# Kernel optimization log

Measured on AMD Instinct MI355X. Metric: run time of the kernel, lower is better.

## Reference

```python
import jax, jax.numpy as jnp
import numpy as np

B, D = 64, 65536   # batch, num default boxes
NEG_POS = 3        # negative:positive mining ratio (init arg)


def _bce_with_logits(x, t):
    # numerically stable elementwise BCE-with-logits (matches torch)
    return jnp.maximum(x, 0.0) - x * t + jnp.log1p(jnp.exp(-jnp.abs(x)))


def _smooth_l1(d):
    ad = jnp.abs(d)
    return jnp.where(ad < 1.0, 0.5 * d * d, ad - 0.5)


def setup_inputs() -> dict:
    key = jax.random.key(0)
    k1, k2, k3, k4 = jax.random.split(key, 4)
    loc_data = jax.random.normal(k1, (B, D, 4), dtype=jnp.float32)
    conf_data = jax.random.normal(k2, (B, D, 1), dtype=jnp.float32)
    loc_t = jax.random.normal(k3, (B, D, 4), dtype=jnp.float32)
    conf_t = (jax.random.uniform(k4, (B, D)) < 0.02).astype(jnp.int32)
    return {"loc_data": loc_data, "conf_data": conf_data,
            "loc_t": loc_t, "conf_t": conf_t}


def reference(loc_data, conf_data, loc_t, conf_t):
    pos = conf_t > 0                                  # [B, D]
    num_pos = pos.sum(axis=1, keepdims=True)          # [B, 1]

    # ---- localization loss: smooth-L1 mean over positive box coords ----
    pf = pos[:, :, None].astype(loc_data.dtype)       # [B, D, 1]
    sl1 = _smooth_l1(loc_data - loc_t) * pf           # [B, D, 4]
    n_loc_elems = pf.sum() * 4.0                      # masked-gather -> mean
    loss_l = sl1.sum() / n_loc_elems

    # ---- confidence loss with hard negative mining ----
    logits = conf_data[:, :, 0]                       # [B, D]
    bce = _bce_with_logits(logits, conf_t.astype(logits.dtype))
    bce_neg = jnp.where(pos, 0.0, bce)                # zero-out positives
    # double argsort -> per-row rank of each element's loss (descending)
    loss_idx = jnp.argsort(-bce_neg, axis=1)          # [B, D]
    idx_rank = jnp.argsort(loss_idx, axis=1)          # [B, D]
    num_neg = jnp.minimum(num_pos * NEG_POS, D)       # [B, 1]
    neg = idx_rank < num_neg                          # top-k hardest negatives
    sel = (pos | neg).astype(logits.dtype)            # [B, D]
    loss_c = (bce * sel).sum() / sel.sum()            # mean over selected

    N = num_pos.sum().astype(logits.dtype)
    return (loss_l / N, loss_c / N)
```

## Files before the change

### kernel.cpp

```cpp
#include <hip/hip_runtime.h>
#include <stdint.h>


#define B_ 64
#define D_ 65536
#define NEGPOS 3
#define BPR 16
#define NBLK (B_ * BPR)
#define CHUNK (D_ / BPR)
#define XC 1.25f
#define HBINS 4096
#define XRANGE 5.0f
#define CJCAP 1024

#define OFF_SL1P     0
#define OFF_BCEP     8192
#define OFF_NP       16384
#define OFF_CC       20480
#define OFF_NEGSUM   24576
#define OFF_KSEL     25088
#define OFF_CNT      25344
#define OFF_CAND     32768

__device__ __forceinline__ void stgF(float* p, float v) {
    __hip_atomic_store(p, v, __ATOMIC_RELAXED, __HIP_MEMORY_SCOPE_AGENT);
}
__device__ __forceinline__ void stgU(unsigned* p, unsigned v) {
    __hip_atomic_store(p, v, __ATOMIC_RELAXED, __HIP_MEMORY_SCOPE_AGENT);
}
__device__ __forceinline__ void stgI(int* p, int v) {
    __hip_atomic_store(p, v, __ATOMIC_RELAXED, __HIP_MEMORY_SCOPE_AGENT);
}
__device__ __forceinline__ void stgD(double* p, double v) {
    __hip_atomic_store(p, v, __ATOMIC_RELAXED, __HIP_MEMORY_SCOPE_AGENT);
}
__device__ __forceinline__ float ldgF(const float* p) {
    return __hip_atomic_load(p, __ATOMIC_RELAXED, __HIP_MEMORY_SCOPE_AGENT);
}
__device__ __forceinline__ unsigned ldgU(const unsigned* p) {
    return __hip_atomic_load(p, __ATOMIC_RELAXED, __HIP_MEMORY_SCOPE_AGENT);
}
__device__ __forceinline__ int ldgI(const int* p) {
    return __hip_atomic_load(p, __ATOMIC_RELAXED, __HIP_MEMORY_SCOPE_AGENT);
}
__device__ __forceinline__ double ldgD(const double* p) {
    return __hip_atomic_load(p, __ATOMIC_RELAXED, __HIP_MEMORY_SCOPE_AGENT);
}

__device__ __forceinline__ float softplus_f(float x) {
    return fmaxf(x, 0.0f) + log1pf(expf(-fabsf(x)));
}

__device__ __forceinline__ int bin_of_x(float x) {
    int b = (int)((x - XC) * ((float)HBINS / XRANGE));
    return max(0, min(HBINS - 1, b));
}

__device__ __forceinline__ float smooth_l1_4(float4 a, float4 b) {
    float s = 0.0f, d, ad;
    d = a.x - b.x; ad = fabsf(d); s += (ad < 1.0f) ? 0.5f * d * d : ad - 0.5f;
    d = a.y - b.y; ad = fabsf(d); s += (ad < 1.0f) ? 0.5f * d * d : ad - 0.5f;
    d = a.z - b.z; ad = fabsf(d); s += (ad < 1.0f) ? 0.5f * d * d : ad - 0.5f;
    d = a.w - b.w; ad = fabsf(d); s += (ad < 1.0f) ? 0.5f * d * d : ad - 0.5f;
    return s;
}

__device__ __forceinline__ double wredD(double v) {
#pragma unroll
    for (int o = 32; o > 0; o >>= 1) v += __shfl_down(v, o, 64);
    return v;
}
__device__ __forceinline__ int wredI(int v) {
#pragma unroll
    for (int o = 32; o > 0; o >>= 1) v += __shfl_down(v, o, 64);
    return v;
}

__device__ __forceinline__ int blockSumI(int v, int* sh) {
    int w = wredI(v);
    const int lane = threadIdx.x & 63, wid = threadIdx.x >> 6;
    __syncthreads();
    if (lane == 0) sh[wid] = w;
    __syncthreads();
    return sh[0] + sh[1] + sh[2] + sh[3];
}

__global__ void __launch_bounds__(256)
mbl_fused(const float4* __restrict__ loc4, const float* __restrict__ conf,
          const float4* __restrict__ loct4, const int* __restrict__ conft,
          unsigned char* __restrict__ ws, float* __restrict__ out)
{
    __shared__ union {
        struct { float lcand[CHUNK]; unsigned short lpos[CHUNK]; } a;
        struct { unsigned hist[HBINS]; float ubuf[CJCAP]; } b;
    } u;
    __shared__ unsigned wtot[4];
    __shared__ double wr[8];
    __shared__ double wrC[4];
    __shared__ int shN[4], shK[4];
    __shared__ unsigned segoff[BPR + 1], sccS[BPR], wsuf[4];
    __shared__ unsigned shJ, shRemJ, shCj, shNP;
    __shared__ int shI[4];
    __shared__ int shLast;

    const int block = blockIdx.x;
    const int row = block >> 4;
    const int base = block * CHUNK;
    const int lane = threadIdx.x & 63, wid = threadIdx.x >> 6;

    {
        const float4* c4 = (const float4*)(conf + base);
        const int4*   t4 = (const int4*)(conft + base);

        float4 xv[4]; int4 tv[4];
#pragma unroll
        for (int it = 0; it < 4; it++) {
            const int g = threadIdx.x + it * 256;
            xv[it] = c4[g];
            tv[it] = t4[g];
        }

        double bcp = 0.0;
        unsigned cntc = 0, cntp = 0;
#pragma unroll
        for (int it = 0; it < 4; it++) {
#pragma unroll
            for (int c = 0; c < 4; c++) {
                float x = (c == 0) ? xv[it].x : (c == 1) ? xv[it].y : (c == 2) ? xv[it].z : xv[it].w;
                int   t = (c == 0) ? tv[it].x : (c == 1) ? tv[it].y : (c == 2) ? tv[it].z : tv[it].w;
                if (t > 0) { cntp++; bcp += (double)(softplus_f(x) - x); }
                else if (x >= XC) cntc++;
            }
        }

        unsigned pk = (cntc << 16) | cntp;
        unsigned incl = pk;
#pragma unroll
        for (int o = 1; o < 64; o <<= 1) {
            unsigned v = __shfl_up(incl, o, 64);
            if (lane >= o) incl += v;
        }
        unsigned excl = incl - pk;
        if (lane == 63) wtot[wid] = incl;
        __syncthreads();
        unsigned wbase = 0;
        for (int w = 0; w < wid; w++) wbase += wtot[w];
        const unsigned tot = wtot[0] + wtot[1] + wtot[2] + wtot[3];
        const unsigned totc = tot >> 16, totp = tot & 0xFFFFu;
        unsigned offc = (excl >> 16) + (wbase >> 16);
        unsigned offp = (excl & 0xFFFFu) + (wbase & 0xFFFFu);

#pragma unroll
        for (int it = 0; it < 4; it++) {
#pragma unroll
            for (int c = 0; c < 4; c++) {
                float x = (c == 0) ? xv[it].x : (c == 1) ? xv[it].y : (c == 2) ? xv[it].z : xv[it].w;
                int   t = (c == 0) ? tv[it].x : (c == 1) ? tv[it].y : (c == 2) ? tv[it].z : tv[it].w;
                const int li = (threadIdx.x + it * 256) * 4 + c;
                if (t > 0) u.a.lpos[offp++] = (unsigned short)li;
                else if (x >= XC) u.a.lcand[offc++] = x;
            }
        }
        __syncthreads();

        float* seg = (float*)(ws + OFF_CAND) + (size_t)block * CHUNK;
        for (unsigned i = threadIdx.x; i < totc; i += 256) stgF(seg + i, u.a.lcand[i]);

        double sl1 = 0.0;
        for (unsigned i = threadIdx.x; i < totp; i += 256) {
            const int e = base + (int)u.a.lpos[i];
            sl1 += (double)smooth_l1_4(loc4[e], loct4[e]);
        }

        double s1 = wredD(sl1), s2 = wredD(bcp);
        if (lane == 0) { wr[wid] = s1; wr[4 + wid] = s2; }
        __syncthreads();
        if (threadIdx.x == 0) {
            stgD((double*)(ws + OFF_SL1P) + block, wr[0] + wr[1] + wr[2] + wr[3]);
            stgD((double*)(ws + OFF_BCEP) + block, wr[4] + wr[5] + wr[6] + wr[7]);
            stgU((unsigned*)(ws + OFF_NP) + block, totp);
            stgU((unsigned*)(ws + OFF_CC) + block, totc);
        }
    }

    __syncthreads();
    if (threadIdx.x == 0) {
        unsigned old = __hip_atomic_fetch_add(
            (unsigned*)(ws + OFF_CNT) + row, 1u,
            __ATOMIC_RELAXED, __HIP_MEMORY_SCOPE_AGENT);
        shLast = (old == BPR - 1) ? 1 : 0;
    }
    __syncthreads();
    if (!shLast) return;

    const unsigned* ccp = (const unsigned*)(ws + OFF_CC) + row * BPR;
    const unsigned* npp = (const unsigned*)(ws + OFF_NP) + row * BPR;

    if (wid == 0) {
        unsigned c = (lane < BPR) ? ldgU(ccp + lane) : 0u;
        unsigned p = (lane < BPR) ? ldgU(npp + lane) : 0u;
        unsigned inc = c;
#pragma unroll
        for (int o = 1; o < BPR; o <<= 1) {
            unsigned v = __shfl_up(inc, o, 64);
            if (lane >= o) inc += v;
        }
        unsigned ptot = p;
#pragma unroll
        for (int o = 1; o < BPR; o <<= 1) ptot += __shfl_down(ptot, o, 64);
        if (lane < BPR) { segoff[lane] = inc - c; sccS[lane] = c; }
        if (lane == BPR - 1) segoff[BPR] = inc;
        if (lane == 0) { shNP = ptot; shCj = 0; }
    }
    __syncthreads();

    const int np = (int)shNP;
    const unsigned n = segoff[BPR];
    long long k = (long long)np * NEGPOS;
    if (k > D_) k = D_;
    long long negs = (long long)D_ - np;
    if (k > negs) k = negs;
    if (threadIdx.x == 0) stgI((int*)(ws + OFF_KSEL) + row, (int)k);

    bool donesum = false;
    bool needfb = false;
    if (k <= 0) {
        if (threadIdx.x == 0) stgD((double*)(ws + OFF_NEGSUM) + row, 0.0);
        donesum = true;
    } else if ((long long)n < k) {
        needfb = true;
    }

    const float* cand = (const float*)(ws + OFF_CAND);

    if (!donesum && !needfb) {
        for (int i = threadIdx.x; i < HBINS; i += 256) u.b.hist[i] = 0;
        __syncthreads();
        const int s = threadIdx.x >> 4, li = threadIdx.x & 15;
        const float* gseg = cand + (size_t)(row * BPR + s) * CHUNK;
        const unsigned cs = sccS[s];
        for (unsigned i = li; i < cs; i += 16)
            atomicAdd(&u.b.hist[bin_of_x(ldgF(gseg + i))], 1u);
        __syncthreads();

        {
            unsigned s16 = 0; const int b0 = threadIdx.x * 16;
#pragma unroll
            for (int i = 0; i < 16; i++) s16 += u.b.hist[b0 + i];
            unsigned suf = s16;
#pragma unroll
            for (int o = 1; o < 64; o <<= 1) {
                unsigned v = __shfl_down(suf, o, 64);
                if (lane + o < 64) suf += v;
            }
            if (lane == 0) wsuf[wid] = suf;
            __syncthreads();
            unsigned add = 0;
            for (int w = wid + 1; w < 4; w++) add += wsuf[w];
            suf += add;
            const unsigned sufx = suf - s16;
            if ((long long)sufx < k && (long long)suf >= k) {
                long long cum = sufx;
                for (int b = b0 + 15; b >= b0; b--) {
                    cum += u.b.hist[b];
                    if (cum >= k) {
                        shJ = (unsigned)b;
                        shRemJ = (unsigned)(k - (cum - (long long)u.b.hist[b]));
                        break;
                    }
                }
            }
        }
        __syncthreads();
        const unsigned J = shJ, remJ = shRemJ;

        double acc = 0.0;
        for (unsigned i = li; i < cs; i += 16) {
            const float x = ldgF(gseg + i);
            const int b = bin_of_x(x);
            if (b > (int)J) acc += (double)softplus_f(x);
            else if (b == (int)J) {
                unsigned p = atomicAdd(&shCj, 1u);
                if (p < CJCAP) u.b.ubuf[p] = x;
            }
        }
        __syncthreads();
        const unsigned cj = shCj;

        if (cj <= CJCAP) {
            for (unsigned i = threadIdx.x; i < cj; i += 256) {
                const float xi = u.b.ubuf[i];
                unsigned r = 0;
                for (unsigned l = 0; l < cj; l++) {
                    const float xl = u.b.ubuf[l];
                    r += (xl > xi || (xl == xi && l < i)) ? 1u : 0u;
                }
                if (r < remJ) acc += (double)softplus_f(xi);
            }
            double t = wredD(acc);
            if (lane == 0) wr[wid] = t;
            __syncthreads();
            if (threadIdx.x == 0)
                stgD((double*)(ws + OFF_NEGSUM) + row, wr[0] + wr[1] + wr[2] + wr[3]);
            donesum = true;
        } else {
            needfb = true;
        }
    }

    if (!donesum && needfb) {
        const float* rowc = conf + row * D_;
        const int*   rowt = conft + row * D_;
        unsigned lo = 0u, hi = 0xFFFFFFFFu;
        for (int it = 0; it < 32; it++) {
            const unsigned mid = lo + ((hi - lo) >> 1);
            unsigned um = (mid & 0x80000000u) ? (mid & 0x7FFFFFFFu) : ~mid;
            float fm = __uint_as_float(um);
            int c = 0;
            for (int i = threadIdx.x; i < D_; i += 256)
                if (rowt[i] <= 0 && rowc[i] > fm) c++;
            const int tot = blockSumI(c, shI);
            if ((long long)tot >= k) lo = mid; else hi = mid;
        }
        unsigned uT = (hi & 0x80000000u) ? (hi & 0x7FFFFFFFu) : ~hi;
        float xT = __uint_as_float(uT);
        int c = 0;
        double acc = 0.0;
        for (int i = threadIdx.x; i < D_; i += 256) {
            if (rowt[i] <= 0) {
                float x = rowc[i];
                if (x > xT) { c++; acc += (double)softplus_f(x); }
            }
        }
        int rem = (int)(k - (long long)blockSumI(c, shI));
        double t = wredD(acc);
        if (lane == 0) wr[wid] = t;
        __syncthreads();
        if (threadIdx.x == 0)
            stgD((double*)(ws + OFF_NEGSUM) + row,
                 wr[0] + wr[1] + wr[2] + wr[3] +
                 (double)rem * (double)softplus_f(xT));
    }

    __syncthreads();
    if (threadIdx.x == 0) {
        unsigned old = __hip_atomic_fetch_add(
            (unsigned*)(ws + OFF_CNT) + B_, 1u,
            __ATOMIC_RELAXED, __HIP_MEMORY_SCOPE_AGENT);
        shLast = (old == B_ - 1) ? 1 : 0;
    }
    __syncthreads();
    if (!shLast) return;

    {
        const double* sl1p = (const double*)(ws + OFF_SL1P);
        const double* bcep = (const double*)(ws + OFF_BCEP);
        const unsigned* npb = (const unsigned*)(ws + OFF_NP);
        const int* kselp = (const int*)(ws + OFF_KSEL);
        const double* nsp = (const double*)(ws + OFF_NEGSUM);

        double a = 0.0, b2 = 0.0, c2 = 0.0;
        int nn = 0, kk = 0;
        for (int i = threadIdx.x; i < NBLK; i += 256) {
            a += ldgD(sl1p + i); b2 += ldgD(bcep + i); nn += (int)ldgU(npb + i);
        }
        if (threadIdx.x < B_) { kk = ldgI(kselp + threadIdx.x); c2 = ldgD(nsp + threadIdx.x); }

        double ra = wredD(a), rb = wredD(b2), rc = wredD(c2);
        int rn = wredI(nn), rk = wredI(kk);
        if (lane == 0) { wr[wid] = ra; wr[4 + wid] = rb; wrC[wid] = rc; shN[wid] = rn; shK[wid] = rk; }
        __syncthreads();
        if (threadIdx.x == 0) {
            double SL1 = wr[0] + wr[1] + wr[2] + wr[3];
            double BCE = wr[4] + wr[5] + wr[6] + wr[7];
            double NSUM = wrC[0] + wrC[1] + wrC[2] + wrC[3];
            double Np = (double)(shN[0] + shN[1] + shN[2] + shN[3]);
            double Kt = (double)(shK[0] + shK[1] + shK[2] + shK[3]);
            double out0 = (Np > 0.0) ? (SL1 / (4.0 * Np)) / Np : 0.0;
            double denom = Np + Kt;
            double out1 = (Np > 0.0 && denom > 0.0) ? ((BCE + NSUM) / denom) / Np : 0.0;
            out[0] = (float)out0;
            out[1] = (float)out1;
        }
    }
}

extern "C" void kernel_launch(void* const* d_in, const int* in_sizes, int n_in,
                              void* d_out, int out_size, void* d_ws, size_t ws_size,
                              hipStream_t stream)
{
    const float4* loc4  = (const float4*)d_in[0];
    const float*  conf  = (const float*)d_in[1];
    const float4* loct4 = (const float4*)d_in[2];
    const int*    conft = (const int*)d_in[3];
    unsigned char* ws = (unsigned char*)d_ws;
    float* out = (float*)d_out;

    hipMemsetAsync(ws + OFF_CNT, 0, (B_ + 1) * sizeof(unsigned), stream);
    mbl_fused<<<dim3(NBLK), dim3(256), 0, stream>>>(loc4, conf, loct4, conft, ws, out);
}
```

Measured before the change: 194.2 us.

## Drop LDS compaction, write candidates directly, vectorize row-reducer and final loads

The first phase no longer compacts candidates and positive indices through shared memory. Positives compute smooth-L1 inline during the scan, and candidate values are stored straight to global scratch. The per-row reducer now loads each segment's candidates into registers with fixed-width coherent vector loads, capped at RCAP per segment, and falls back to the slow row path if any segment exceeds that cap. The final reducer uses vectorized cache-bypassing loads, and shared memory shrinks so four blocks fit per CU. The risks are scattered per-element global stores and divergent gathers of loc data, plus fallback when candidate counts per segment exceed the cap.

```diff
diff --git a/kernel.cpp b/kernel.cpp
--- a/kernel.cpp
+++ b/kernel.cpp
@@ -12,15 +12,20 @@
 #define HBINS 4096
 #define XRANGE 5.0f
 #define CJCAP 1024
-
-#define OFF_SL1P     0
-#define OFF_BCEP     8192
-#define OFF_NP       16384
-#define OFF_CC       20480
-#define OFF_NEGSUM   24576
-#define OFF_KSEL     25088
-#define OFF_CNT      25344
-#define OFF_CAND     32768
+#define RQ 10
+#define RCAP (16 * RQ * 4)
+
+typedef unsigned long long ull;
+typedef unsigned uint32x4 __attribute__((ext_vector_type(4)));
+
+#define OFF_SL1P   0
+#define OFF_BCEP   8192
+#define OFF_NP     16384
+#define OFF_CC     20480
+#define OFF_NEGSUM 24576
+#define OFF_KSEL   25088
+#define OFF_CNT    25344
+#define OFF_CAND   32768
 
 __device__ __forceinline__ void stgF(float* p, float v) {
     __hip_atomic_store(p, v, __ATOMIC_RELAXED, __HIP_MEMORY_SCOPE_AGENT);
@@ -34,17 +39,50 @@
 __device__ __forceinline__ void stgD(double* p, double v) {
     __hip_atomic_store(p, v, __ATOMIC_RELAXED, __HIP_MEMORY_SCOPE_AGENT);
 }
-__device__ __forceinline__ float ldgF(const float* p) {
-    return __hip_atomic_load(p, __ATOMIC_RELAXED, __HIP_MEMORY_SCOPE_AGENT);
-}
 __device__ __forceinline__ unsigned ldgU(const unsigned* p) {
     return __hip_atomic_load(p, __ATOMIC_RELAXED, __HIP_MEMORY_SCOPE_AGENT);
 }
-__device__ __forceinline__ int ldgI(const int* p) {
-    return __hip_atomic_load(p, __ATOMIC_RELAXED, __HIP_MEMORY_SCOPE_AGENT);
-}
-__device__ __forceinline__ double ldgD(const double* p) {
-    return __hip_atomic_load(p, __ATOMIC_RELAXED, __HIP_MEMORY_SCOPE_AGENT);
+
+__device__ __forceinline__ void ldg160B_sc(const void* p,
+        uint32x4& a0, uint32x4& a1, uint32x4& a2, uint32x4& a3, uint32x4& a4,
+        uint32x4& a5, uint32x4& a6, uint32x4& a7, uint32x4& a8, uint32x4& a9) {
+    asm volatile(
+        "global_load_dwordx4 %0, %10, off sc0 sc1\n\t"
+        "global_load_dwordx4 %1, %10, off offset:16 sc0 sc1\n\t"
+        "global_load_dwordx4 %2, %10, off offset:32 sc0 sc1\n\t"
+        "global_load_dwordx4 %3, %10, off offset:48 sc0 sc1\n\t"
+        "global_load_dwordx4 %4, %10, off offset:64 sc0 sc1\n\t"
+        "global_load_dwordx4 %5, %10, off offset:80 sc0 sc1\n\t"
+        "global_load_dwordx4 %6, %10, off offset:96 sc0 sc1\n\t"
+        "global_load_dwordx4 %7, %10, off offset:112 sc0 sc1\n\t"
+        "global_load_dwordx4 %8, %10, off offset:128 sc0 sc1\n\t"
+        "global_load_dwordx4 %9, %10, off offset:144 sc0 sc1\n\t"
+        "s_waitcnt vmcnt(0)"
+        : "=&v"(a0), "=&v"(a1), "=&v"(a2), "=&v"(a3), "=&v"(a4),
+          "=&v"(a5), "=&v"(a6), "=&v"(a7), "=&v"(a8), "=&v"(a9)
+        : "v"(p)
+        : "memory");
+}
+__device__ __forceinline__ void ldg32B_sc(const void* p, uint32x4& a, uint32x4& b) {
+    asm volatile(
+        "global_load_dwordx4 %0, %2, off sc0 sc1\n\t"
+        "global_load_dwordx4 %1, %2, off offset:16 sc0 sc1\n\t"
+        "s_waitcnt vmcnt(0)"
+        : "=&v"(a), "=&v"(b)
+        : "v"(p)
+        : "memory");
+}
+__device__ __forceinline__ void ldg16B_sc(const void* p, uint32x4& a) {
+    asm volatile(
+        "global_load_dwordx4 %0, %1, off sc0 sc1\n\t"
+        "s_waitcnt vmcnt(0)"
+        : "=&v"(a)
+        : "v"(p)
+        : "memory");
+}
+
+__device__ __forceinline__ double mkD(unsigned lo, unsigned hi) {
+    return __longlong_as_double(((ull)hi << 32) | lo);
 }
 
 __device__ __forceinline__ float softplus_f(float x) {
@@ -85,22 +123,29 @@
     return sh[0] + sh[1] + sh[2] + sh[3];
 }
 
-__global__ void __launch_bounds__(256)
+#define H1(XU, OFS) do { if (idx0 + (OFS) < cs) \
+        atomicAdd(&hist[bin_of_x(__uint_as_float(XU))], 1u); } while (0)
+#define H4(RV, Q) do { H1((RV).x, (Q)*4+0); H1((RV).y, (Q)*4+1); \
+                       H1((RV).z, (Q)*4+2); H1((RV).w, (Q)*4+3); } while (0)
+#define S1(XU, OFS) do { if (idx0 + (OFS) < cs) { \
+        const float x_ = __uint_as_float(XU); const int b_ = bin_of_x(x_); \
+        if (b_ > (int)J) acc += (double)softplus_f(x_); \
+        else if (b_ == (int)J) { unsigned sl_ = atomicAdd(&shCj, 1u); \
+            if (sl_ < CJCAP) ubuf[sl_] = x_; } } } while (0)
+#define S4(RV, Q) do { S1((RV).x, (Q)*4+0); S1((RV).y, (Q)*4+1); \
+                       S1((RV).z, (Q)*4+2); S1((RV).w, (Q)*4+3); } while (0)
+
+__global__ void __launch_bounds__(256, 4)
 mbl_fused(const float4* __restrict__ loc4, const float* __restrict__ conf,
           const float4* __restrict__ loct4, const int* __restrict__ conft,
           unsigned char* __restrict__ ws, float* __restrict__ out)
 {
-    __shared__ union {
-        struct { float lcand[CHUNK]; unsigned short lpos[CHUNK]; } a;
-        struct { unsigned hist[HBINS]; float ubuf[CJCAP]; } b;
-    } u;
-    __shared__ unsigned wtot[4];
-    __shared__ double wr[8];
-    __shared__ double wrC[4];
-    __shared__ int shN[4], shK[4];
-    __shared__ unsigned segoff[BPR + 1], sccS[BPR], wsuf[4];
-    __shared__ unsigned shJ, shRemJ, shCj, shNP;
-    __shared__ int shI[4];
+    __shared__ unsigned hist[HBINS];
+    __shared__ float ubuf[CJCAP];
+    __shared__ unsigned wtot[4], wsuf[4], sccS[BPR];
+    __shared__ double wrD[8], wrC[4];
+    __shared__ int shI[4], shN[4], shK[4];
+    __shared__ unsigned shJ, shRemJ, shNP, shT, shCj, shFB;
     __shared__ int shLast;
 
     const int block = blockIdx.x;
@@ -120,7 +165,7 @@
             tv[it] = t4[g];
         }
 
-        double bcp = 0.0;
+        double bcp = 0.0, sl1 = 0.0;
         unsigned cntc = 0, cntp = 0;
 #pragma unroll
         for (int it = 0; it < 4; it++) {
@@ -128,57 +173,48 @@
             for (int c = 0; c < 4; c++) {
                 float x = (c == 0) ? xv[it].x : (c == 1) ? xv[it].y : (c == 2) ? xv[it].z : xv[it].w;
                 int   t = (c == 0) ? tv[it].x : (c == 1) ? tv[it].y : (c == 2) ? tv[it].z : tv[it].w;
-                if (t > 0) { cntp++; bcp += (double)(softplus_f(x) - x); }
-                else if (x >= XC) cntc++;
-            }
-        }
-
-        unsigned pk = (cntc << 16) | cntp;
-        unsigned incl = pk;
+                if (t > 0) {
+                    cntp++;
+                    bcp += (double)(softplus_f(x) - x);
+                    const int e = base + (threadIdx.x + it * 256) * 4 + c;
+                    sl1 += (double)smooth_l1_4(loc4[e], loct4[e]);
+                } else if (x >= XC) cntc++;
+            }
+        }
+
+        unsigned incl = cntc;
 #pragma unroll
         for (int o = 1; o < 64; o <<= 1) {
             unsigned v = __shfl_up(incl, o, 64);
             if (lane >= o) incl += v;
         }
-        unsigned excl = incl - pk;
+        unsigned excl = incl - cntc;
         if (lane == 63) wtot[wid] = incl;
         __syncthreads();
         unsigned wbase = 0;
         for (int w = 0; w < wid; w++) wbase += wtot[w];
-        const unsigned tot = wtot[0] + wtot[1] + wtot[2] + wtot[3];
-        const unsigned totc = tot >> 16, totp = tot & 0xFFFFu;
-        unsigned offc = (excl >> 16) + (wbase >> 16);
-        unsigned offp = (excl & 0xFFFFu) + (wbase & 0xFFFFu);
-
+        const unsigned totc = wtot[0] + wtot[1] + wtot[2] + wtot[3];
+        unsigned offc = excl + wbase;
+
+        float* seg = (float*)(ws + OFF_CAND) + (size_t)block * CHUNK;
 #pragma unroll
         for (int it = 0; it < 4; it++) {
 #pragma unroll
             for (int c = 0; c < 4; c++) {
                 float x = (c == 0) ? xv[it].x : (c == 1) ? xv[it].y : (c == 2) ? xv[it].z : xv[it].w;
                 int   t = (c == 0) ? tv[it].x : (c == 1) ? tv[it].y : (c == 2) ? tv[it].z : tv[it].w;
-                const int li = (threadIdx.x + it * 256) * 4 + c;
-                if (t > 0) u.a.lpos[offp++] = (unsigned short)li;
-                else if (x >= XC) u.a.lcand[offc++] = x;
-            }
-        }
-        __syncthreads();
-
-        float* seg = (float*)(ws + OFF_CAND) + (size_t)block * CHUNK;
-        for (unsigned i = threadIdx.x; i < totc; i += 256) stgF(seg + i, u.a.lcand[i]);
-
-        double sl1 = 0.0;
-        for (unsigned i = threadIdx.x; i < totp; i += 256) {
-            const int e = base + (int)u.a.lpos[i];
-            sl1 += (double)smooth_l1_4(loc4[e], loct4[e]);
+                if (t <= 0 && x >= XC) stgF(seg + offc++, x);
+            }
         }
 
         double s1 = wredD(sl1), s2 = wredD(bcp);
-        if (lane == 0) { wr[wid] = s1; wr[4 + wid] = s2; }
+        int tp = wredI((int)cntp);
+        if (lane == 0) { wrD[wid] = s1; wrD[4 + wid] = s2; shN[wid] = tp; }
         __syncthreads();
         if (threadIdx.x == 0) {
-            stgD((double*)(ws + OFF_SL1P) + block, wr[0] + wr[1] + wr[2] + wr[3]);
-            stgD((double*)(ws + OFF_BCEP) + block, wr[4] + wr[5] + wr[6] + wr[7]);
-            stgU((unsigned*)(ws + OFF_NP) + block, totp);
+            stgD((double*)(ws + OFF_SL1P) + block, wrD[0] + wrD[1] + wrD[2] + wrD[3]);
+            stgD((double*)(ws + OFF_BCEP) + block, wrD[4] + wrD[5] + wrD[6] + wrD[7]);
+            stgU((unsigned*)(ws + OFF_NP) + block, (unsigned)(shN[0] + shN[1] + shN[2] + shN[3]));
             stgU((unsigned*)(ws + OFF_CC) + block, totc);
         }
     }
@@ -193,81 +229,85 @@
     __syncthreads();
     if (!shLast) return;
 
-    const unsigned* ccp = (const unsigned*)(ws + OFF_CC) + row * BPR;
-    const unsigned* npp = (const unsigned*)(ws + OFF_NP) + row * BPR;
-
-    if (wid == 0) {
-        unsigned c = (lane < BPR) ? ldgU(ccp + lane) : 0u;
-        unsigned p = (lane < BPR) ? ldgU(npp + lane) : 0u;
-        unsigned inc = c;
-#pragma unroll
-        for (int o = 1; o < BPR; o <<= 1) {
-            unsigned v = __shfl_up(inc, o, 64);
-            if (lane >= o) inc += v;
-        }
-        unsigned ptot = p;
-#pragma unroll
-        for (int o = 1; o < BPR; o <<= 1) ptot += __shfl_down(ptot, o, 64);
-        if (lane < BPR) { segoff[lane] = inc - c; sccS[lane] = c; }
-        if (lane == BPR - 1) segoff[BPR] = inc;
-        if (lane == 0) { shNP = ptot; shCj = 0; }
-    }
-    __syncthreads();
+    {
+        const unsigned* ccp = (const unsigned*)(ws + OFF_CC) + row * BPR;
+        const unsigned* npp = (const unsigned*)(ws + OFF_NP) + row * BPR;
+        if (wid == 0) {
+            unsigned c = (lane < BPR) ? ldgU(ccp + lane) : 0u;
+            unsigned p = (lane < BPR) ? ldgU(npp + lane) : 0u;
+            if (lane < BPR) sccS[lane] = c;
+            unsigned ctot = c, ptot = p;
+#pragma unroll
+            for (int o = 1; o < BPR; o <<= 1) {
+                ctot += __shfl_down(ctot, o, 64);
+                ptot += __shfl_down(ptot, o, 64);
+            }
+            ull ov = __ballot(lane < BPR && c > RCAP);
+            if (lane == 0) {
+                shT = ctot; shNP = ptot;
+                shFB = (ov != 0ull) ? 1u : 0u;
+                shCj = 0;
+            }
+        }
+        __syncthreads();
+    }
 
     const int np = (int)shNP;
-    const unsigned n = segoff[BPR];
     long long k = (long long)np * NEGPOS;
     if (k > D_) k = D_;
     long long negs = (long long)D_ - np;
     if (k > negs) k = negs;
     if (threadIdx.x == 0) stgI((int*)(ws + OFF_KSEL) + row, (int)k);
 
-    bool donesum = false;
-    bool needfb = false;
+    bool done = false;
     if (k <= 0) {
         if (threadIdx.x == 0) stgD((double*)(ws + OFF_NEGSUM) + row, 0.0);
-        donesum = true;
-    } else if ((long long)n < k) {
-        needfb = true;
-    }
-
-    const float* cand = (const float*)(ws + OFF_CAND);
-
-    if (!donesum && !needfb) {
-        for (int i = threadIdx.x; i < HBINS; i += 256) u.b.hist[i] = 0;
-        __syncthreads();
+        done = true;
+    }
+    bool fb = !done && (shFB || (long long)shT < k);
+
+    if (!done && !fb) {
         const int s = threadIdx.x >> 4, li = threadIdx.x & 15;
-        const float* gseg = cand + (size_t)(row * BPR + s) * CHUNK;
         const unsigned cs = sccS[s];
-        for (unsigned i = li; i < cs; i += 16)
-            atomicAdd(&u.b.hist[bin_of_x(ldgF(gseg + i))], 1u);
-        __syncthreads();
-
-        {
-            unsigned s16 = 0; const int b0 = threadIdx.x * 16;
-#pragma unroll
-            for (int i = 0; i < 16; i++) s16 += u.b.hist[b0 + i];
-            unsigned suf = s16;
-#pragma unroll
-            for (int o = 1; o < 64; o <<= 1) {
-                unsigned v = __shfl_down(suf, o, 64);
-                if (lane + o < 64) suf += v;
-            }
-            if (lane == 0) wsuf[wid] = suf;
-            __syncthreads();
-            unsigned add = 0;
-            for (int w = wid + 1; w < 4; w++) add += wsuf[w];
-            suf += add;
-            const unsigned sufx = suf - s16;
-            if ((long long)sufx < k && (long long)suf >= k) {
-                long long cum = sufx;
-                for (int b = b0 + 15; b >= b0; b--) {
-                    cum += u.b.hist[b];
-                    if (cum >= k) {
-                        shJ = (unsigned)b;
-                        shRemJ = (unsigned)(k - (cum - (long long)u.b.hist[b]));
-                        break;
-                    }
+        const unsigned idx0 = (unsigned)li * (RQ * 4);
+        const float* cand = (const float*)(ws + OFF_CAND);
+        const unsigned char* segp =
+            (const unsigned char*)(cand + (size_t)(row * BPR + s) * CHUNK)
+            + (size_t)li * (RQ * 16);
+
+        uint32x4 r0, r1, r2, r3, r4, r5, r6, r7, r8, r9;
+        ldg160B_sc(segp, r0, r1, r2, r3, r4, r5, r6, r7, r8, r9);
+
+        for (int i = threadIdx.x; i < HBINS; i += 256) hist[i] = 0;
+        __syncthreads();
+        H4(r0, 0); H4(r1, 1); H4(r2, 2); H4(r3, 3); H4(r4, 4);
+        H4(r5, 5); H4(r6, 6); H4(r7, 7); H4(r8, 8); H4(r9, 9);
+        __syncthreads();
+
+        unsigned s16 = 0;
+        const int b0i = threadIdx.x * 16;
+#pragma unroll
+        for (int j = 0; j < 16; j++) s16 += hist[b0i + j];
+        unsigned suf = s16;
+#pragma unroll
+        for (int o = 1; o < 64; o <<= 1) {
+            unsigned v = __shfl_down(suf, o, 64);
+            if (lane + o < 64) suf += v;
+        }
+        if (lane == 0) wsuf[wid] = suf;
+        __syncthreads();
+        unsigned addw = 0;
+        for (int w = wid + 1; w < 4; w++) addw += wsuf[w];
+        suf += addw;
+        const unsigned sufx = suf - s16;
+        if ((long long)sufx < k && (long long)suf >= k) {
+            long long cum = sufx;
+            for (int j = 15; j >= 0; j--) {
+                cum += hist[b0i + j];
+                if (cum >= k) {
+                    shJ = (unsigned)(b0i + j);
+                    shRemJ = (unsigned)(k - (cum - (long long)hist[b0i + j]));
+                    break;
                 }
             }
         }
@@ -275,40 +315,32 @@
         const unsigned J = shJ, remJ = shRemJ;
 
         double acc = 0.0;
-        for (unsigned i = li; i < cs; i += 16) {
-            const float x = ldgF(gseg + i);
-            const int b = bin_of_x(x);
-            if (b > (int)J) acc += (double)softplus_f(x);
-            else if (b == (int)J) {
-                unsigned p = atomicAdd(&shCj, 1u);
-                if (p < CJCAP) u.b.ubuf[p] = x;
-            }
-        }
+        S4(r0, 0); S4(r1, 1); S4(r2, 2); S4(r3, 3); S4(r4, 4);
+        S4(r5, 5); S4(r6, 6); S4(r7, 7); S4(r8, 8); S4(r9, 9);
         __syncthreads();
         const unsigned cj = shCj;
 
         if (cj <= CJCAP) {
             for (unsigned i = threadIdx.x; i < cj; i += 256) {
-                const float xi = u.b.ubuf[i];
+                const float xi = ubuf[i];
                 unsigned r = 0;
                 for (unsigned l = 0; l < cj; l++) {
-                    const float xl = u.b.ubuf[l];
+                    const float xl = ubuf[l];
                     r += (xl > xi || (xl == xi && l < i)) ? 1u : 0u;
                 }
                 if (r < remJ) acc += (double)softplus_f(xi);
             }
             double t = wredD(acc);
-            if (lane == 0) wr[wid] = t;
+            if (lane == 0) wrD[wid] = t;
             __syncthreads();
             if (threadIdx.x == 0)
-                stgD((double*)(ws + OFF_NEGSUM) + row, wr[0] + wr[1] + wr[2] + wr[3]);
-            donesum = true;
-        } else {
-            needfb = true;
-        }
-    }
-
-    if (!donesum && needfb) {
+                stgD((double*)(ws + OFF_NEGSUM) + row,
+                     wrD[0] + wrD[1] + wrD[2] + wrD[3]);
+            done = true;
+        } else fb = true;
+    }
+
+    if (!done && fb) {
         const float* rowc = conf + row * D_;
         const int*   rowt = conft + row * D_;
         unsigned lo = 0u, hi = 0xFFFFFFFFu;
@@ -334,11 +366,11 @@
         }
         int rem = (int)(k - (long long)blockSumI(c, shI));
         double t = wredD(acc);
-        if (lane == 0) wr[wid] = t;
+        if (lane == 0) wrD[wid] = t;
         __syncthreads();
         if (threadIdx.x == 0)
             stgD((double*)(ws + OFF_NEGSUM) + row,
-                 wr[0] + wr[1] + wr[2] + wr[3] +
+                 wrD[0] + wrD[1] + wrD[2] + wrD[3] +
                  (double)rem * (double)softplus_f(xT));
     }
 
@@ -353,26 +385,29 @@
     if (!shLast) return;
 
     {
-        const double* sl1p = (const double*)(ws + OFF_SL1P);
-        const double* bcep = (const double*)(ws + OFF_BCEP);
-        const unsigned* npb = (const unsigned*)(ws + OFF_NP);
-        const int* kselp = (const int*)(ws + OFF_KSEL);
-        const double* nsp = (const double*)(ws + OFF_NEGSUM);
-
-        double a = 0.0, b2 = 0.0, c2 = 0.0;
-        int nn = 0, kk = 0;
-        for (int i = threadIdx.x; i < NBLK; i += 256) {
-            a += ldgD(sl1p + i); b2 += ldgD(bcep + i); nn += (int)ldgU(npb + i);
-        }
-        if (threadIdx.x < B_) { kk = ldgI(kselp + threadIdx.x); c2 = ldgD(nsp + threadIdx.x); }
+        uint32x4 pa, pb, qa, qb, na;
+        ldg32B_sc(ws + OFF_SL1P + (size_t)threadIdx.x * 32, pa, pb);
+        ldg32B_sc(ws + OFF_BCEP + (size_t)threadIdx.x * 32, qa, qb);
+        ldg16B_sc(ws + OFF_NP + (size_t)threadIdx.x * 16, na);
+        double a  = mkD(pa.x, pa.y) + mkD(pa.z, pa.w) + mkD(pb.x, pb.y) + mkD(pb.z, pb.w);
+        double b2 = mkD(qa.x, qa.y) + mkD(qa.z, qa.w) + mkD(qb.x, qb.y) + mkD(qb.z, qb.w);
+        int nn = (int)(na.x + na.y + na.z + na.w);
+        double c2 = 0.0; int kk = 0;
+        if (threadIdx.x < 16) {
+            uint32x4 ca, cb, ka;
+            ldg32B_sc(ws + OFF_NEGSUM + (size_t)threadIdx.x * 32, ca, cb);
+            ldg16B_sc(ws + OFF_KSEL + (size_t)threadIdx.x * 16, ka);
+            c2 = mkD(ca.x, ca.y) + mkD(ca.z, ca.w) + mkD(cb.x, cb.y) + mkD(cb.z, cb.w);
+            kk = (int)ka.x + (int)ka.y + (int)ka.z + (int)ka.w;
+        }
 
         double ra = wredD(a), rb = wredD(b2), rc = wredD(c2);
         int rn = wredI(nn), rk = wredI(kk);
-        if (lane == 0) { wr[wid] = ra; wr[4 + wid] = rb; wrC[wid] = rc; shN[wid] = rn; shK[wid] = rk; }
+        if (lane == 0) { wrD[wid] = ra; wrD[4 + wid] = rb; wrC[wid] = rc; shN[wid] = rn; shK[wid] = rk; }
         __syncthreads();
         if (threadIdx.x == 0) {
-            double SL1 = wr[0] + wr[1] + wr[2] + wr[3];
-            double BCE = wr[4] + wr[5] + wr[6] + wr[7];
+            double SL1 = wrD[0] + wrD[1] + wrD[2] + wrD[3];
+            double BCE = wrD[4] + wrD[5] + wrD[6] + wrD[7];
             double NSUM = wrC[0] + wrC[1] + wrC[2] + wrC[3];
             double Np = (double)(shN[0] + shN[1] + shN[2] + shN[3]);
             double Kt = (double)(shK[0] + shK[1] + shK[2] + shK[3]);
```

Result: slower. 227.8 us (+17.3%).
